# Kernel optimization log

Measured on AMD Instinct MI355X. Metric: run time of the kernel, lower is better.

## Reference

```python
import jax, jax.numpy as jnp
import numpy as np

N_NODES = 100000
NODE_DIM = 64
IN_DIM_V = 128
N_LAYERS = 4
N_CLASSES = 40
N_EDGES = 1600000
LEAKY_SLOPE = 0.2
BN_EPS = 1e-5


def setup_inputs() -> dict:
    key = jax.random.key(0)
    ks = jax.random.split(key, 12)
    V = jax.random.normal(ks[0], (N_NODES, IN_DIM_V), dtype=jnp.float32)
    src = jax.random.randint(ks[1], (N_EDGES,), 0, N_NODES, dtype=jnp.int64 if jax.config.jax_enable_x64 else jnp.int32)
    dst = jax.random.randint(ks[2], (N_EDGES,), 0, N_NODES, dtype=jnp.int64 if jax.config.jax_enable_x64 else jnp.int32)
    s_in = 1.0 / np.sqrt(IN_DIM_V)
    s_h = 1.0 / np.sqrt(NODE_DIM)
    W_in = jax.random.normal(ks[3], (IN_DIM_V, NODE_DIM), dtype=jnp.float32) * s_in
    b_in = jnp.zeros((NODE_DIM,), jnp.float32)
    W_l = jax.random.normal(ks[4], (N_LAYERS, NODE_DIM, NODE_DIM), dtype=jnp.float32) * s_h
    b_l = jnp.zeros((N_LAYERS, NODE_DIM), jnp.float32)
    gamma = jnp.ones((N_LAYERS, NODE_DIM), jnp.float32)
    beta = jnp.zeros((N_LAYERS, NODE_DIM), jnp.float32)
    W_out = jax.random.normal(ks[5], (NODE_DIM, N_CLASSES), dtype=jnp.float32) * s_h
    b_out = jnp.zeros((N_CLASSES,), jnp.float32)
    return {"V": V, "src": src, "dst": dst, "W_in": W_in, "b_in": b_in,
            "W_l": W_l, "b_l": b_l, "gamma": gamma, "beta": beta,
            "W_out": W_out, "b_out": b_out}


def _batchnorm(x, g, b):
    # BatchNorm1d in training mode: biased variance over the node axis
    m = jnp.mean(x, axis=0)
    v = jnp.mean(jnp.square(x - m), axis=0)
    return (x - m) * jax.lax.rsqrt(v + BN_EPS) * g + b


def reference(V, src, dst, W_in, b_in, W_l, b_l, gamma, beta, W_out, b_out):
    N = V.shape[0]
    ones = jnp.ones((src.shape[0],), V.dtype)
    deg_out = jax.ops.segment_sum(ones, src, num_segments=N)
    deg_in = jax.ops.segment_sum(ones, dst, num_segments=N)
    norm_src = jax.lax.rsqrt(jnp.clip(deg_out, 1.0))[:, None]  # [N,1]
    norm_dst = jax.lax.rsqrt(jnp.clip(deg_in, 1.0))[:, None]

    # trans_input: linear embedding in_dim_V -> node_dim
    h = V @ W_in + b_in  # [N, node_dim]

    for l in range(N_LAYERS):
        h_in = h
        # dropout p=0 / eval mode -> identity
        # GraphConv norm='both': D^{-1/2} A D^{-1/2} X W + b
        m = h * norm_src                                      # [N, d]
        agg = jax.ops.segment_sum(m[src], dst, num_segments=N)  # gather-scatter over edges
        agg = agg * norm_dst
        hc = agg @ W_l[l] + b_l[l]
        hc = _batchnorm(hc, gamma[l], beta[l])
        hc = jnp.where(hc >= 0, hc, LEAKY_SLOPE * hc)
        h = hc + h_in  # residual (cell index hard-wired to 1 in source)

    logits = h @ W_out + b_out  # trans_output: node_dim -> n_classes
    return jax.nn.log_softmax(logits, axis=1)
```

## Files before the change

kernel.cpp:

```cpp
#include <hip/hip_runtime.h>
#include <math.h>


#define LEAKY_SLOPE 0.2f
#define BN_EPS 1e-5f
#define DEG_CAP 48

__device__ __forceinline__ unsigned short f2bf(float f) {
  unsigned int x = __float_as_uint(f);
  unsigned int r = (x + 0x7FFFu + ((x >> 16) & 1u)) >> 16;
  return (unsigned short)r;
}
__device__ __forceinline__ float bf2f(unsigned short u) {
  return __uint_as_float((unsigned int)u << 16);
}

__global__ __launch_bounds__(256, 8)
void hist_kernel(const int* __restrict__ src, int* __restrict__ cnt_src, int E, int N) {
  int bid = blockIdx.x;
  int w = bid & 7;
  int chunk = (N + 7) >> 3;
  int lo = w * chunk;
  int hi = min(lo + chunk, N);
  int i = (bid >> 3) * blockDim.x + threadIdx.x;
  int stride = (gridDim.x >> 3) * blockDim.x;
  for (; i < E; i += stride) {
    int s = src[i];
    if (s >= lo && s < hi) atomicAdd(&cnt_src[s], 1);
  }
}

__global__ __launch_bounds__(256, 8)
void fill_kernel(const int* __restrict__ src, const int* __restrict__ dst,
                 int* __restrict__ cnt_dst, int* __restrict__ bucket, int E, int N) {
  int bid = blockIdx.x;
  int w = bid & 7;
  int chunk = (N + 7) >> 3;
  int lo = w * chunk;
  int hi = min(lo + chunk, N);
  int i = (bid >> 3) * blockDim.x + threadIdx.x;
  int stride = (gridDim.x >> 3) * blockDim.x;
  for (; i < E; i += stride) {
    int d = dst[i];
    if (d >= lo && d < hi) {
      int pos = atomicAdd(&cnt_dst[d], 1);
      if (pos < DEG_CAP) bucket[d * DEG_CAP + pos] = src[i];
    }
  }
}

__global__ __launch_bounds__(256, 8)
void norms_kernel(const int* __restrict__ cnt_src, const int* __restrict__ cnt_dst,
                  float* __restrict__ norm_src, float* __restrict__ norm_dst, int N) {
  int i = blockIdx.x * blockDim.x + threadIdx.x;
  if (i < N) {
    norm_src[i] = rsqrtf(fmaxf((float)cnt_src[i], 1.0f));
    norm_dst[i] = rsqrtf(fmaxf((float)cnt_dst[i], 1.0f));
  }
}

__global__ __launch_bounds__(256) __attribute__((amdgpu_waves_per_eu(3, 4)))
void input_gemm_kernel(const float* __restrict__ V, const float* __restrict__ W_in,
                       const float* __restrict__ b_in, const float* __restrict__ norm_src,
                       float* __restrict__ h, unsigned short* __restrict__ hs, int N) {
  __shared__ __align__(16) float sW[128][64];
  __shared__ __align__(16) float sA[32][132];
  int tid = threadIdx.x;
  int c0 = (tid & 15) * 4;
  int rp = tid >> 4;
  int base = blockIdx.x * 32;

  float4 b4 = *(const float4*)&b_in[c0];

  #pragma unroll
  for (int it = 0; it < 8; it++) {
    int i = tid + it * 256;
    int r = i >> 4, cc = (i & 15) * 4;
    *(float4*)&sW[r][cc] = *(const float4*)&W_in[r * 64 + cc];
  }
  #pragma unroll
  for (int it = 0; it < 4; it++) {
    int i = tid + it * 256;
    int r = i >> 5, cc = (i & 31) * 4;
    int n = base + r;
    float4 v = make_float4(0.f, 0.f, 0.f, 0.f);
    if (n < N) v = *(const float4*)&V[(size_t)n * 128 + cc];
    *(float4*)&sA[r][cc] = v;
  }
  __syncthreads();

  int r0 = rp * 2, r1 = rp * 2 + 1;
  float acc0[4] = {0.f, 0.f, 0.f, 0.f};
  float acc1[4] = {0.f, 0.f, 0.f, 0.f};
  #pragma unroll 4
  for (int d0 = 0; d0 < 128; d0 += 4) {
    float4 wr0 = *(const float4*)&sW[d0 + 0][c0];
    float4 wr1 = *(const float4*)&sW[d0 + 1][c0];
    float4 wr2 = *(const float4*)&sW[d0 + 2][c0];
    float4 wr3 = *(const float4*)&sW[d0 + 3][c0];
    float4 a0 = *(const float4*)&sA[r0][d0];
    float4 a1 = *(const float4*)&sA[r1][d0];
    acc0[0] += a0.x * wr0.x + a0.y * wr1.x + a0.z * wr2.x + a0.w * wr3.x;
    acc0[1] += a0.x * wr0.y + a0.y * wr1.y + a0.z * wr2.y + a0.w * wr3.y;
    acc0[2] += a0.x * wr0.z + a0.y * wr1.z + a0.z * wr2.z + a0.w * wr3.z;
    acc0[3] += a0.x * wr0.w + a0.y * wr1.w + a0.z * wr2.w + a0.w * wr3.w;
    acc1[0] += a1.x * wr0.x + a1.y * wr1.x + a1.z * wr2.x + a1.w * wr3.x;
    acc1[1] += a1.x * wr0.y + a1.y * wr1.y + a1.z * wr2.y + a1.w * wr3.y;
    acc1[2] += a1.x * wr0.z + a1.y * wr1.z + a1.z * wr2.z + a1.w * wr3.z;
    acc1[3] += a1.x * wr0.w + a1.y * wr1.w + a1.z * wr2.w + a1.w * wr3.w;
  }

  int n0 = base + r0, n1 = base + r1;
  if (n0 < N) {
    float4 o = make_float4(acc0[0] + b4.x, acc0[1] + b4.y, acc0[2] + b4.z, acc0[3] + b4.w);
    *(float4*)&h[(size_t)n0 * 64 + c0] = o;
    float ns = norm_src[n0];
    ushort4 s = make_ushort4(f2bf(o.x * ns), f2bf(o.y * ns), f2bf(o.z * ns), f2bf(o.w * ns));
    *(ushort4*)&hs[(size_t)n0 * 64 + c0] = s;
  }
  if (n1 < N) {
    float4 o = make_float4(acc1[0] + b4.x, acc1[1] + b4.y, acc1[2] + b4.z, acc1[3] + b4.w);
    *(float4*)&h[(size_t)n1 * 64 + c0] = o;
    float ns = norm_src[n1];
    ushort4 s = make_ushort4(f2bf(o.x * ns), f2bf(o.y * ns), f2bf(o.z * ns), f2bf(o.w * ns));
    *(ushort4*)&hs[(size_t)n1 * 64 + c0] = s;
  }
}

__global__ __launch_bounds__(256, 8)
void agg_kernel(const unsigned short* __restrict__ hs, const float* __restrict__ norm_dst,
                const int* __restrict__ cnt_dst, const int* __restrict__ bucket,
                float* __restrict__ agg, int N) {
  int wid = __builtin_amdgcn_readfirstlane(blockIdx.x * 4 + (threadIdx.x >> 6));
  int lane = threadIdx.x & 63;
  if (wid >= N) return;
  int len = cnt_dst[wid];
  float nd = norm_dst[wid];
  const int* bkt = bucket + wid * DEG_CAP;
  float a0=0.f,a1=0.f,a2=0.f,a3=0.f,a4=0.f,a5=0.f,a6=0.f,a7=0.f;
  for (int j = 0; j < len; j += 8) {
    int s0=0,s1=0,s2=0,s3=0,s4=0,s5=0,s6=0,s7=0;
    if (j + 0 < len) s0 = bkt[j + 0];
    if (j + 1 < len) s1 = bkt[j + 1];
    if (j + 2 < len) s2 = bkt[j + 2];
    if (j + 3 < len) s3 = bkt[j + 3];
    if (j + 4 < len) s4 = bkt[j + 4];
    if (j + 5 < len) s5 = bkt[j + 5];
    if (j + 6 < len) s6 = bkt[j + 6];
    if (j + 7 < len) s7 = bkt[j + 7];
    unsigned short h0=0,h1=0,h2=0,h3=0,h4=0,h5=0,h6=0,h7=0;
    if (j + 0 < len) h0 = hs[(size_t)s0 * 64 + lane];
    if (j + 1 < len) h1 = hs[(size_t)s1 * 64 + lane];
    if (j + 2 < len) h2 = hs[(size_t)s2 * 64 + lane];
    if (j + 3 < len) h3 = hs[(size_t)s3 * 64 + lane];
    if (j + 4 < len) h4 = hs[(size_t)s4 * 64 + lane];
    if (j + 5 < len) h5 = hs[(size_t)s5 * 64 + lane];
    if (j + 6 < len) h6 = hs[(size_t)s6 * 64 + lane];
    if (j + 7 < len) h7 = hs[(size_t)s7 * 64 + lane];
    if (j + 0 < len) a0 += bf2f(h0);
    if (j + 1 < len) a1 += bf2f(h1);
    if (j + 2 < len) a2 += bf2f(h2);
    if (j + 3 < len) a3 += bf2f(h3);
    if (j + 4 < len) a4 += bf2f(h4);
    if (j + 5 < len) a5 += bf2f(h5);
    if (j + 6 < len) a6 += bf2f(h6);
    if (j + 7 < len) a7 += bf2f(h7);
  }
  float acc = ((a0 + a1) + (a2 + a3)) + ((a4 + a5) + (a6 + a7));
  agg[(size_t)wid * 64 + lane] = acc * nd;
}

__global__ __launch_bounds__(256) __attribute__((amdgpu_waves_per_eu(4, 4)))
void gemm_stats_kernel(const float* __restrict__ agg, const float* __restrict__ W,
                       const float* __restrict__ b, float* __restrict__ hc,
                       float* __restrict__ stats, int N) {
  __shared__ __align__(16) float sW[64][64];
  __shared__ __align__(16) float sA[64][68];
  int tid = threadIdx.x;
  int lane = tid & 63;
  int wv = tid >> 6;
  int cg = lane & 15;
  int ng = lane >> 4;
  int nrow0 = wv * 16 + ng * 4;
  int base = blockIdx.x * 64;

  #pragma unroll
  for (int it = 0; it < 4; it++) {
    int i = tid + it * 256;
    int r = i >> 4, c4 = (i & 15) * 4;
    *(float4*)&sW[r][c4] = *(const float4*)&W[r * 64 + c4];
  }
  #pragma unroll
  for (int it = 0; it < 4; it++) {
    int i = tid + it * 256;
    int r = i >> 4, c4 = (i & 15) * 4;
    int n = base + r;
    float4 v = make_float4(0.f, 0.f, 0.f, 0.f);
    if (n < N) v = *(const float4*)&agg[(size_t)n * 64 + c4];
    *(float4*)&sA[r][c4] = v;
  }
  __syncthreads();

  float4 b4 = *(const float4*)&b[cg * 4];

  float acc[4][4];
  #pragma unroll
  for (int i = 0; i < 4; i++)
    #pragma unroll
    for (int c = 0; c < 4; c++) acc[i][c] = 0.f;

  #pragma unroll 4
  for (int d0 = 0; d0 < 64; d0 += 4) {
    float4 wr0 = *(const float4*)&sW[d0 + 0][cg * 4];
    float4 wr1 = *(const float4*)&sW[d0 + 1][cg * 4];
    float4 wr2 = *(const float4*)&sW[d0 + 2][cg * 4];
    float4 wr3 = *(const float4*)&sW[d0 + 3][cg * 4];
    #pragma unroll
    for (int i = 0; i < 4; i++) {
      float4 av = *(const float4*)&sA[nrow0 + i][d0];
      acc[i][0] += av.x * wr0.x + av.y * wr1.x + av.z * wr2.x + av.w * wr3.x;
      acc[i][1] += av.x * wr0.y + av.y * wr1.y + av.z * wr2.y + av.w * wr3.y;
      acc[i][2] += av.x * wr0.z + av.y * wr1.z + av.z * wr2.z + av.w * wr3.z;
      acc[i][3] += av.x * wr0.w + av.y * wr1.w + av.z * wr2.w + av.w * wr3.w;
    }
  }

  float st_s0=0.f,st_s1=0.f,st_s2=0.f,st_s3=0.f;
  float st_q0=0.f,st_q1=0.f,st_q2=0.f,st_q3=0.f;
  #pragma unroll
  for (int i = 0; i < 4; i++) {
    int n = base + nrow0 + i;
    if (n < N) {
      float4 o;
      o.x = acc[i][0] + b4.x; o.y = acc[i][1] + b4.y;
      o.z = acc[i][2] + b4.z; o.w = acc[i][3] + b4.w;
      *(float4*)&hc[(size_t)n * 64 + cg * 4] = o;
      st_s0 += o.x; st_s1 += o.y; st_s2 += o.z; st_s3 += o.w;
      st_q0 += o.x * o.x; st_q1 += o.y * o.y;
      st_q2 += o.z * o.z; st_q3 += o.w * o.w;
    }
  }

  __syncthreads();
  int rr = wv * 4 + ng;
  *(float4*)&sA[rr][cg * 4]      = make_float4(st_s0, st_s1, st_s2, st_s3);
  *(float4*)&sA[16 + rr][cg * 4] = make_float4(st_q0, st_q1, st_q2, st_q3);
  __syncthreads();
  if (tid < 64) {
    float s = 0.f, q = 0.f;
    #pragma unroll
    for (int r = 0; r < 16; r++) { s += sA[r][tid]; q += sA[16 + r][tid]; }
    atomicAdd(&stats[tid], s);
    atomicAdd(&stats[64 + tid], q);
  }
}

__global__ __launch_bounds__(256, 8)
void apply_kernel(const float* __restrict__ hc, const float* __restrict__ stats,
                  const float* __restrict__ gamma, const float* __restrict__ beta,
                  const float* __restrict__ norm_src, float* __restrict__ h,
                  unsigned short* __restrict__ hs, int N, int write_hs) {
  __shared__ float s_scale[64];
  __shared__ float s_shift[64];
  int tid = threadIdx.x;
  if (tid < 64) {
    float s = stats[tid];
    float ss = stats[64 + tid];
    float invN = 1.0f / (float)N;
    float mean = s * invN;
    float var = fmaxf(ss * invN - mean * mean, 0.0f);
    float scale = gamma[tid] * rsqrtf(var + BN_EPS);
    s_scale[tid] = scale;
    s_shift[tid] = beta[tid] - mean * scale;
  }
  __syncthreads();
  int total4 = N * 16;
  int i = blockIdx.x * blockDim.x + threadIdx.x;
  int stride = gridDim.x * blockDim.x;
  for (; i < total4; i += stride) {
    float4 v = ((const float4*)hc)[i];
    float4 r = ((const float4*)h)[i];
    int cb = (i * 4) & 63;
    int n = i >> 4;
    float o0 = v.x * s_scale[cb + 0] + s_shift[cb + 0];
    float o1 = v.y * s_scale[cb + 1] + s_shift[cb + 1];
    float o2 = v.z * s_scale[cb + 2] + s_shift[cb + 2];
    float o3 = v.w * s_scale[cb + 3] + s_shift[cb + 3];
    o0 = (o0 >= 0.f) ? o0 : LEAKY_SLOPE * o0;
    o1 = (o1 >= 0.f) ? o1 : LEAKY_SLOPE * o1;
    o2 = (o2 >= 0.f) ? o2 : LEAKY_SLOPE * o2;
    o3 = (o3 >= 0.f) ? o3 : LEAKY_SLOPE * o3;
    float4 oh;
    oh.x = o0 + r.x; oh.y = o1 + r.y; oh.z = o2 + r.z; oh.w = o3 + r.w;
    ((float4*)h)[i] = oh;
    if (write_hs) {
      float nsc = norm_src[n];
      ushort4 os = make_ushort4(f2bf(oh.x * nsc), f2bf(oh.y * nsc),
                                f2bf(oh.z * nsc), f2bf(oh.w * nsc));
      ((ushort4*)hs)[i] = os;
    }
  }
}

__global__ __launch_bounds__(256, 4)
void out_kernel(const float* __restrict__ h, const float* __restrict__ W_out,
                const float* __restrict__ b_out, float* __restrict__ out, int N) {
  __shared__ float sWoT[40][65];
  int tid = threadIdx.x;
  for (int i = tid; i < 2560; i += 256) {
    int d = i / 40;
    int c = i - d * 40;
    sWoT[c][d] = W_out[i];
  }
  __syncthreads();
  int gw = (int)((blockIdx.x * blockDim.x + tid) >> 6);
  int nw = (int)((gridDim.x * blockDim.x) >> 6);
  int lane = tid & 63;
  int cc = (lane < 40) ? lane : 39;
  float bias = (lane < 40) ? b_out[lane] : 0.f;
  const float* wrow = &sWoT[cc][0];
  for (int n = gw; n < N; n += nw) {
    int nsg = __builtin_amdgcn_readfirstlane(n);
    const float* hrow = h + (size_t)nsg * 64;
    float acc = bias;
    #pragma unroll
    for (int d = 0; d < 64; d++) acc += hrow[d] * wrow[d];
    float lg = (lane < 40) ? acc : -INFINITY;
    float m = lg;
    #pragma unroll
    for (int off = 32; off; off >>= 1) m = fmaxf(m, __shfl_xor(m, off));
    float e = (lane < 40) ? expf(acc - m) : 0.f;
    float s = e;
    #pragma unroll
    for (int off = 32; off; off >>= 1) s += __shfl_xor(s, off);
    float lse = m + logf(s);
    if (lane < 40) out[(size_t)nsg * 40 + lane] = acc - lse;
  }
}

extern "C" void kernel_launch(void* const* d_in, const int* in_sizes, int n_in,
                              void* d_out, int out_size, void* d_ws, size_t ws_size,
                              hipStream_t stream) {
  const float* V     = (const float*)d_in[0];
  const int*   src   = (const int*)d_in[1];
  const int*   dst   = (const int*)d_in[2];
  const float* W_in  = (const float*)d_in[3];
  const float* b_in  = (const float*)d_in[4];
  const float* W_l   = (const float*)d_in[5];
  const float* b_l   = (const float*)d_in[6];
  const float* gamma = (const float*)d_in[7];
  const float* beta  = (const float*)d_in[8];
  const float* W_out = (const float*)d_in[9];
  const float* b_out = (const float*)d_in[10];
  float* out = (float*)d_out;

  const int N = in_sizes[0] / 128;
  const int E = in_sizes[1];
  const int NL = 4;

  char* p = (char*)d_ws;
  auto alloc = [&](size_t bytes) {
    void* r = (void*)p;
    p += (bytes + 255) & ~(size_t)255;
    return r;
  };
  float*          h       = (float*)alloc((size_t)N * 64 * 4);
  float*          agg     = (float*)alloc((size_t)N * 64 * 4);
  float*          hc      = (float*)alloc((size_t)N * 64 * 4);
  unsigned short* hs      = (unsigned short*)alloc((size_t)N * 64 * 2);
  int*            bucket  = (int*)alloc((size_t)N * DEG_CAP * 4);
  int*            cnt_src = (int*)alloc((size_t)N * 4);
  int*            cnt_dst = (int*)alloc((size_t)N * 4);
  float*          nrm_src = (float*)alloc((size_t)N * 4);
  float*          nrm_dst = (float*)alloc((size_t)N * 4);
  float*          stats   = (float*)alloc(128 * 4);
  (void)ws_size;

  hipMemsetAsync(cnt_src, 0, (size_t)N * 4, stream);
  hipMemsetAsync(cnt_dst, 0, (size_t)N * 4, stream);

  hist_kernel<<<2048, 256, 0, stream>>>(src, cnt_src, E, N);
  fill_kernel<<<2048, 256, 0, stream>>>(src, dst, cnt_dst, bucket, E, N);
  norms_kernel<<<(N + 255) / 256, 256, 0, stream>>>(cnt_src, cnt_dst, nrm_src, nrm_dst, N);

  input_gemm_kernel<<<(N + 31) / 32, 256, 0, stream>>>(V, W_in, b_in, nrm_src, h, hs, N);

  for (int l = 0; l < NL; l++) {
    agg_kernel<<<(N + 3) / 4, 256, 0, stream>>>(hs, nrm_dst, cnt_dst, bucket, agg, N);
    hipMemsetAsync(stats, 0, 128 * 4, stream);
    gemm_stats_kernel<<<(N + 63) / 64, 256, 0, stream>>>(agg, W_l + (size_t)l * 64 * 64,
                                                         b_l + (size_t)l * 64, hc, stats, N);
    apply_kernel<<<2048, 256, 0, stream>>>(hc, stats, gamma + (size_t)l * 64,
                                           beta + (size_t)l * 64, nrm_src, h, hs, N,
                                           (l < NL - 1) ? 1 : 0);
  }

  out_kernel<<<1024, 256, 0, stream>>>(h, W_out, b_out, out, N);
}
```

Before: 923.7 us.

## Fuse hist/fill, last apply into output, persistent GEMMs, drop stats memsets

Merges the source-degree histogram and destination bucket fill into one pass over the edge arrays. The final BatchNorm, LeakyReLU and residual step is folded into the output projection and log-softmax kernel, so h is not written back after the last layer. The input and layer GEMMs become grid-stride persistent kernels with 1024 blocks, which amortizes the weight loads into shared memory and cuts the number of stats atomics. The per-layer memsets are replaced by one zeroing of a per-layer stats buffer inside norms_kernel. In exchange, the fused fill does both the src and dst atomics inside each partition pass, and the persistent loops add extra __syncthreads.

```diff
diff --git a/kernel.cpp b/kernel.cpp
--- a/kernel.cpp
+++ b/kernel.cpp
@@ -16,7 +16,9 @@
 }
 
 __global__ __launch_bounds__(256, 8)
-void hist_kernel(const int* __restrict__ src, int* __restrict__ cnt_src, int E, int N) {
+void fill_hist_kernel(const int* __restrict__ src, const int* __restrict__ dst,
+                      int* __restrict__ cnt_src, int* __restrict__ cnt_dst,
+                      int* __restrict__ bucket, int E, int N) {
   int bid = blockIdx.x;
   int w = bid & 7;
   int chunk = (N + 7) >> 3;
@@ -26,33 +28,26 @@
   int stride = (gridDim.x >> 3) * blockDim.x;
   for (; i < E; i += stride) {
     int s = src[i];
+    int d = dst[i];
     if (s >= lo && s < hi) atomicAdd(&cnt_src[s], 1);
-  }
-}
-
-__global__ __launch_bounds__(256, 8)
-void fill_kernel(const int* __restrict__ src, const int* __restrict__ dst,
-                 int* __restrict__ cnt_dst, int* __restrict__ bucket, int E, int N) {
-  int bid = blockIdx.x;
-  int w = bid & 7;
-  int chunk = (N + 7) >> 3;
-  int lo = w * chunk;
-  int hi = min(lo + chunk, N);
-  int i = (bid >> 3) * blockDim.x + threadIdx.x;
-  int stride = (gridDim.x >> 3) * blockDim.x;
-  for (; i < E; i += stride) {
-    int d = dst[i];
     if (d >= lo && d < hi) {
       int pos = atomicAdd(&cnt_dst[d], 1);
-      if (pos < DEG_CAP) bucket[d * DEG_CAP + pos] = src[i];
+      if (pos < DEG_CAP) bucket[d * DEG_CAP + pos] = s;
     }
   }
 }
 
 __global__ __launch_bounds__(256, 8)
 void norms_kernel(const int* __restrict__ cnt_src, const int* __restrict__ cnt_dst,
-                  float* __restrict__ norm_src, float* __restrict__ norm_dst, int N) {
+                  float* __restrict__ norm_src, float* __restrict__ norm_dst,
+                  float* __restrict__ stats, int N) {
   int i = blockIdx.x * blockDim.x + threadIdx.x;
+  if (blockIdx.x == 0) {
+    if (threadIdx.x < 256) {
+      stats[threadIdx.x] = 0.f;
+      stats[256 + threadIdx.x] = 0.f;
+    }
+  }
   if (i < N) {
     norm_src[i] = rsqrtf(fmaxf((float)cnt_src[i], 1.0f));
     norm_dst[i] = rsqrtf(fmaxf((float)cnt_dst[i], 1.0f));
@@ -68,7 +63,6 @@
   int tid = threadIdx.x;
   int c0 = (tid & 15) * 4;
   int rp = tid >> 4;
-  int base = blockIdx.x * 32;
 
   float4 b4 = *(const float4*)&b_in[c0];
 
@@ -78,52 +72,56 @@
     int r = i >> 4, cc = (i & 15) * 4;
     *(float4*)&sW[r][cc] = *(const float4*)&W_in[r * 64 + cc];
   }
-  #pragma unroll
-  for (int it = 0; it < 4; it++) {
-    int i = tid + it * 256;
-    int r = i >> 5, cc = (i & 31) * 4;
-    int n = base + r;
-    float4 v = make_float4(0.f, 0.f, 0.f, 0.f);
-    if (n < N) v = *(const float4*)&V[(size_t)n * 128 + cc];
-    *(float4*)&sA[r][cc] = v;
-  }
-  __syncthreads();
-
-  int r0 = rp * 2, r1 = rp * 2 + 1;
-  float acc0[4] = {0.f, 0.f, 0.f, 0.f};
-  float acc1[4] = {0.f, 0.f, 0.f, 0.f};
-  #pragma unroll 4
-  for (int d0 = 0; d0 < 128; d0 += 4) {
-    float4 wr0 = *(const float4*)&sW[d0 + 0][c0];
-    float4 wr1 = *(const float4*)&sW[d0 + 1][c0];
-    float4 wr2 = *(const float4*)&sW[d0 + 2][c0];
-    float4 wr3 = *(const float4*)&sW[d0 + 3][c0];
-    float4 a0 = *(const float4*)&sA[r0][d0];
-    float4 a1 = *(const float4*)&sA[r1][d0];
-    acc0[0] += a0.x * wr0.x + a0.y * wr1.x + a0.z * wr2.x + a0.w * wr3.x;
-    acc0[1] += a0.x * wr0.y + a0.y * wr1.y + a0.z * wr2.y + a0.w * wr3.y;
-    acc0[2] += a0.x * wr0.z + a0.y * wr1.z + a0.z * wr2.z + a0.w * wr3.z;
-    acc0[3] += a0.x * wr0.w + a0.y * wr1.w + a0.z * wr2.w + a0.w * wr3.w;
-    acc1[0] += a1.x * wr0.x + a1.y * wr1.x + a1.z * wr2.x + a1.w * wr3.x;
-    acc1[1] += a1.x * wr0.y + a1.y * wr1.y + a1.z * wr2.y + a1.w * wr3.y;
-    acc1[2] += a1.x * wr0.z + a1.y * wr1.z + a1.z * wr2.z + a1.w * wr3.z;
-    acc1[3] += a1.x * wr0.w + a1.y * wr1.w + a1.z * wr2.w + a1.w * wr3.w;
-  }
-
-  int n0 = base + r0, n1 = base + r1;
-  if (n0 < N) {
-    float4 o = make_float4(acc0[0] + b4.x, acc0[1] + b4.y, acc0[2] + b4.z, acc0[3] + b4.w);
-    *(float4*)&h[(size_t)n0 * 64 + c0] = o;
-    float ns = norm_src[n0];
-    ushort4 s = make_ushort4(f2bf(o.x * ns), f2bf(o.y * ns), f2bf(o.z * ns), f2bf(o.w * ns));
-    *(ushort4*)&hs[(size_t)n0 * 64 + c0] = s;
-  }
-  if (n1 < N) {
-    float4 o = make_float4(acc1[0] + b4.x, acc1[1] + b4.y, acc1[2] + b4.z, acc1[3] + b4.w);
-    *(float4*)&h[(size_t)n1 * 64 + c0] = o;
-    float ns = norm_src[n1];
-    ushort4 s = make_ushort4(f2bf(o.x * ns), f2bf(o.y * ns), f2bf(o.z * ns), f2bf(o.w * ns));
-    *(ushort4*)&hs[(size_t)n1 * 64 + c0] = s;
+
+  for (int base = blockIdx.x * 32; base < N; base += gridDim.x * 32) {
+    __syncthreads();
+    #pragma unroll
+    for (int it = 0; it < 4; it++) {
+      int i = tid + it * 256;
+      int r = i >> 5, cc = (i & 31) * 4;
+      int n = base + r;
+      float4 v = make_float4(0.f, 0.f, 0.f, 0.f);
+      if (n < N) v = *(const float4*)&V[(size_t)n * 128 + cc];
+      *(float4*)&sA[r][cc] = v;
+    }
+    __syncthreads();
+
+    int r0 = rp * 2, r1 = rp * 2 + 1;
+    float acc0[4] = {0.f, 0.f, 0.f, 0.f};
+    float acc1[4] = {0.f, 0.f, 0.f, 0.f};
+    #pragma unroll 4
+    for (int d0 = 0; d0 < 128; d0 += 4) {
+      float4 wr0 = *(const float4*)&sW[d0 + 0][c0];
+      float4 wr1 = *(const float4*)&sW[d0 + 1][c0];
+      float4 wr2 = *(const float4*)&sW[d0 + 2][c0];
+      float4 wr3 = *(const float4*)&sW[d0 + 3][c0];
+      float4 a0 = *(const float4*)&sA[r0][d0];
+      float4 a1 = *(const float4*)&sA[r1][d0];
+      acc0[0] += a0.x * wr0.x + a0.y * wr1.x + a0.z * wr2.x + a0.w * wr3.x;
+      acc0[1] += a0.x * wr0.y + a0.y * wr1.y + a0.z * wr2.y + a0.w * wr3.y;
+      acc0[2] += a0.x * wr0.z + a0.y * wr1.z + a0.z * wr2.z + a0.w * wr3.z;
+      acc0[3] += a0.x * wr0.w + a0.y * wr1.w + a0.z * wr2.w + a0.w * wr3.w;
+      acc1[0] += a1.x * wr0.x + a1.y * wr1.x + a1.z * wr2.x + a1.w * wr3.x;
+      acc1[1] += a1.x * wr0.y + a1.y * wr1.y + a1.z * wr2.y + a1.w * wr3.y;
+      acc1[2] += a1.x * wr0.z + a1.y * wr1.z + a1.z * wr2.z + a1.w * wr3.z;
+      acc1[3] += a1.x * wr0.w + a1.y * wr1.w + a1.z * wr2.w + a1.w * wr3.w;
+    }
+
+    int n0 = base + r0, n1 = base + r1;
+    if (n0 < N) {
+      float4 o = make_float4(acc0[0] + b4.x, acc0[1] + b4.y, acc0[2] + b4.z, acc0[3] + b4.w);
+      *(float4*)&h[(size_t)n0 * 64 + c0] = o;
+      float ns = norm_src[n0];
+      ushort4 s = make_ushort4(f2bf(o.x * ns), f2bf(o.y * ns), f2bf(o.z * ns), f2bf(o.w * ns));
+      *(ushort4*)&hs[(size_t)n0 * 64 + c0] = s;
+    }
+    if (n1 < N) {
+      float4 o = make_float4(acc1[0] + b4.x, acc1[1] + b4.y, acc1[2] + b4.z, acc1[3] + b4.w);
+      *(float4*)&h[(size_t)n1 * 64 + c0] = o;
+      float ns = norm_src[n1];
+      ushort4 s = make_ushort4(f2bf(o.x * ns), f2bf(o.y * ns), f2bf(o.z * ns), f2bf(o.w * ns));
+      *(ushort4*)&hs[(size_t)n1 * 64 + c0] = s;
+    }
   }
 }
 
@@ -182,7 +180,6 @@
   int cg = lane & 15;
   int ng = lane >> 4;
   int nrow0 = wv * 16 + ng * 4;
-  int base = blockIdx.x * 64;
 
   #pragma unroll
   for (int it = 0; it < 4; it++) {
@@ -190,54 +187,59 @@
     int r = i >> 4, c4 = (i & 15) * 4;
     *(float4*)&sW[r][c4] = *(const float4*)&W[r * 64 + c4];
   }
-  #pragma unroll
-  for (int it = 0; it < 4; it++) {
-    int i = tid + it * 256;
-    int r = i >> 4, c4 = (i & 15) * 4;
-    int n = base + r;
-    float4 v = make_float4(0.f, 0.f, 0.f, 0.f);
-    if (n < N) v = *(const float4*)&agg[(size_t)n * 64 + c4];
-    *(float4*)&sA[r][c4] = v;
-  }
-  __syncthreads();
 
   float4 b4 = *(const float4*)&b[cg * 4];
-
-  float acc[4][4];
-  #pragma unroll
-  for (int i = 0; i < 4; i++)
-    #pragma unroll
-    for (int c = 0; c < 4; c++) acc[i][c] = 0.f;
-
-  #pragma unroll 4
-  for (int d0 = 0; d0 < 64; d0 += 4) {
-    float4 wr0 = *(const float4*)&sW[d0 + 0][cg * 4];
-    float4 wr1 = *(const float4*)&sW[d0 + 1][cg * 4];
-    float4 wr2 = *(const float4*)&sW[d0 + 2][cg * 4];
-    float4 wr3 = *(const float4*)&sW[d0 + 3][cg * 4];
-    #pragma unroll
-    for (int i = 0; i < 4; i++) {
-      float4 av = *(const float4*)&sA[nrow0 + i][d0];
-      acc[i][0] += av.x * wr0.x + av.y * wr1.x + av.z * wr2.x + av.w * wr3.x;
-      acc[i][1] += av.x * wr0.y + av.y * wr1.y + av.z * wr2.y + av.w * wr3.y;
-      acc[i][2] += av.x * wr0.z + av.y * wr1.z + av.z * wr2.z + av.w * wr3.z;
-      acc[i][3] += av.x * wr0.w + av.y * wr1.w + av.z * wr2.w + av.w * wr3.w;
-    }
-  }
 
   float st_s0=0.f,st_s1=0.f,st_s2=0.f,st_s3=0.f;
   float st_q0=0.f,st_q1=0.f,st_q2=0.f,st_q3=0.f;
-  #pragma unroll
-  for (int i = 0; i < 4; i++) {
-    int n = base + nrow0 + i;
-    if (n < N) {
-      float4 o;
-      o.x = acc[i][0] + b4.x; o.y = acc[i][1] + b4.y;
-      o.z = acc[i][2] + b4.z; o.w = acc[i][3] + b4.w;
-      *(float4*)&hc[(size_t)n * 64 + cg * 4] = o;
-      st_s0 += o.x; st_s1 += o.y; st_s2 += o.z; st_s3 += o.w;
-      st_q0 += o.x * o.x; st_q1 += o.y * o.y;
-      st_q2 += o.z * o.z; st_q3 += o.w * o.w;
+
+  for (int base = blockIdx.x * 64; base < N; base += gridDim.x * 64) {
+    __syncthreads();
+    #pragma unroll
+    for (int it = 0; it < 4; it++) {
+      int i = tid + it * 256;
+      int r = i >> 4, c4 = (i & 15) * 4;
+      int n = base + r;
+      float4 v = make_float4(0.f, 0.f, 0.f, 0.f);
+      if (n < N) v = *(const float4*)&agg[(size_t)n * 64 + c4];
+      *(float4*)&sA[r][c4] = v;
+    }
+    __syncthreads();
+
+    float acc[4][4];
+    #pragma unroll
+    for (int i = 0; i < 4; i++)
+      #pragma unroll
+      for (int c = 0; c < 4; c++) acc[i][c] = 0.f;
+
+    #pragma unroll 4
+    for (int d0 = 0; d0 < 64; d0 += 4) {
+      float4 wr0 = *(const float4*)&sW[d0 + 0][cg * 4];
+      float4 wr1 = *(const float4*)&sW[d0 + 1][cg * 4];
+      float4 wr2 = *(const float4*)&sW[d0 + 2][cg * 4];
+      float4 wr3 = *(const float4*)&sW[d0 + 3][cg * 4];
+      #pragma unroll
+      for (int i = 0; i < 4; i++) {
+        float4 av = *(const float4*)&sA[nrow0 + i][d0];
+        acc[i][0] += av.x * wr0.x + av.y * wr1.x + av.z * wr2.x + av.w * wr3.x;
+        acc[i][1] += av.x * wr0.y + av.y * wr1.y + av.z * wr2.y + av.w * wr3.y;
+        acc[i][2] += av.x * wr0.z + av.y * wr1.z + av.z * wr2.z + av.w * wr3.z;
+        acc[i][3] += av.x * wr0.w + av.y * wr1.w + av.z * wr2.w + av.w * wr3.w;
+      }
+    }
+
+    #pragma unroll
+    for (int i = 0; i < 4; i++) {
+      int n = base + nrow0 + i;
+      if (n < N) {
+        float4 o;
+        o.x = acc[i][0] + b4.x; o.y = acc[i][1] + b4.y;
+        o.z = acc[i][2] + b4.z; o.w = acc[i][3] + b4.w;
+        *(float4*)&hc[(size_t)n * 64 + cg * 4] = o;
+        st_s0 += o.x; st_s1 += o.y; st_s2 += o.z; st_s3 += o.w;
+        st_q0 += o.x * o.x; st_q1 += o.y * o.y;
+        st_q2 += o.z * o.z; st_q3 += o.w * o.w;
+      }
     }
   }
 
@@ -259,7 +261,7 @@
 void apply_kernel(const float* __restrict__ hc, const float* __restrict__ stats,
                   const float* __restrict__ gamma, const float* __restrict__ beta,
                   const float* __restrict__ norm_src, float* __restrict__ h,
-                  unsigned short* __restrict__ hs, int N, int write_hs) {
+                  unsigned short* __restrict__ hs, int N) {
   __shared__ float s_scale[64];
   __shared__ float s_shift[64];
   int tid = threadIdx.x;
@@ -293,38 +295,55 @@
     float4 oh;
     oh.x = o0 + r.x; oh.y = o1 + r.y; oh.z = o2 + r.z; oh.w = o3 + r.w;
     ((float4*)h)[i] = oh;
-    if (write_hs) {
-      float nsc = norm_src[n];
-      ushort4 os = make_ushort4(f2bf(oh.x * nsc), f2bf(oh.y * nsc),
-                                f2bf(oh.z * nsc), f2bf(oh.w * nsc));
-      ((ushort4*)hs)[i] = os;
-    }
+    float nsc = norm_src[n];
+    ushort4 os = make_ushort4(f2bf(oh.x * nsc), f2bf(oh.y * nsc),
+                              f2bf(oh.z * nsc), f2bf(oh.w * nsc));
+    ((ushort4*)hs)[i] = os;
   }
 }
 
 __global__ __launch_bounds__(256, 4)
-void out_kernel(const float* __restrict__ h, const float* __restrict__ W_out,
-                const float* __restrict__ b_out, float* __restrict__ out, int N) {
+void out_fused_kernel(const float* __restrict__ hc, const float* __restrict__ stats,
+                      const float* __restrict__ gamma, const float* __restrict__ beta,
+                      const float* __restrict__ h, const float* __restrict__ W_out,
+                      const float* __restrict__ b_out, float* __restrict__ out, int N) {
   __shared__ float sWoT[40][65];
+  __shared__ float s_scale[64];
+  __shared__ float s_shift[64];
+  __shared__ float sH[4][64];
   int tid = threadIdx.x;
   for (int i = tid; i < 2560; i += 256) {
     int d = i / 40;
     int c = i - d * 40;
     sWoT[c][d] = W_out[i];
   }
+  if (tid < 64) {
+    float s = stats[tid];
+    float ss = stats[64 + tid];
+    float invN = 1.0f / (float)N;
+    float mean = s * invN;
+    float var = fmaxf(ss * invN - mean * mean, 0.0f);
+    float scale = gamma[tid] * rsqrtf(var + BN_EPS);
+    s_scale[tid] = scale;
+    s_shift[tid] = beta[tid] - mean * scale;
+  }
   __syncthreads();
-  int gw = (int)((blockIdx.x * blockDim.x + tid) >> 6);
-  int nw = (int)((gridDim.x * blockDim.x) >> 6);
+  int wv = tid >> 6;
   int lane = tid & 63;
+  int gw = blockIdx.x * 4 + wv;
+  int nw = gridDim.x * 4;
   int cc = (lane < 40) ? lane : 39;
   float bias = (lane < 40) ? b_out[lane] : 0.f;
-  const float* wrow = &sWoT[cc][0];
   for (int n = gw; n < N; n += nw) {
-    int nsg = __builtin_amdgcn_readfirstlane(n);
-    const float* hrow = h + (size_t)nsg * 64;
+    float v = hc[(size_t)n * 64 + lane];
+    float o = v * s_scale[lane] + s_shift[lane];
+    o = (o >= 0.f) ? o : LEAKY_SLOPE * o;
+    float oh = o + h[(size_t)n * 64 + lane];
+    sH[wv][lane] = oh;
+    __builtin_amdgcn_wave_barrier();
     float acc = bias;
     #pragma unroll
-    for (int d = 0; d < 64; d++) acc += hrow[d] * wrow[d];
+    for (int d = 0; d < 64; d++) acc += sH[wv][d] * sWoT[cc][d];
     float lg = (lane < 40) ? acc : -INFINITY;
     float m = lg;
     #pragma unroll
@@ -334,7 +353,8 @@
     #pragma unroll
     for (int off = 32; off; off >>= 1) s += __shfl_xor(s, off);
     float lse = m + logf(s);
-    if (lane < 40) out[(size_t)nsg * 40 + lane] = acc - lse;
+    if (lane < 40) out[(size_t)n * 40 + lane] = acc - lse;
+    __builtin_amdgcn_wave_barrier();
   }
 }
 
@@ -373,27 +393,30 @@
   int*            cnt_dst = (int*)alloc((size_t)N * 4);
   float*          nrm_src = (float*)alloc((size_t)N * 4);
   float*          nrm_dst = (float*)alloc((size_t)N * 4);
-  float*          stats   = (float*)alloc(128 * 4);
+  float*          stats   = (float*)alloc(4 * 128 * 4);
   (void)ws_size;
 
   hipMemsetAsync(cnt_src, 0, (size_t)N * 4, stream);
   hipMemsetAsync(cnt_dst, 0, (size_t)N * 4, stream);
 
-  hist_kernel<<<2048, 256, 0, stream>>>(src, cnt_src, E, N);
-  fill_kernel<<<2048, 256, 0, stream>>>(src, dst, cnt_dst, bucket, E, N);
-  norms_kernel<<<(N + 255) / 256, 256, 0, stream>>>(cnt_src, cnt_dst, nrm_src, nrm_dst, N);
-
-  input_gemm_kernel<<<(N + 31) / 32, 256, 0, stream>>>(V, W_in, b_in, nrm_src, h, hs, N);
+  fill_hist_kernel<<<2048, 256, 0, stream>>>(src, dst, cnt_src, cnt_dst, bucket, E, N);
+  norms_kernel<<<(N + 255) / 256, 256, 0, stream>>>(cnt_src, cnt_dst, nrm_src, nrm_dst,
+                                                    stats, N);
+
+  input_gemm_kernel<<<1024, 256, 0, stream>>>(V, W_in, b_in, nrm_src, h, hs, N);
 
   for (int l = 0; l < NL; l++) {
+    float* statl = stats + (size_t)l * 128;
     agg_kernel<<<(N + 3) / 4, 256, 0, stream>>>(hs, nrm_dst, cnt_dst, bucket, agg, N);
-    hipMemsetAsync(stats, 0, 128 * 4, stream);
-    gemm_stats_kernel<<<(N + 63) / 64, 256, 0, stream>>>(agg, W_l + (size_t)l * 64 * 64,
-                                                         b_l + (size_t)l * 64, hc, stats, N);
-    apply_kernel<<<2048, 256, 0, stream>>>(hc, stats, gamma + (size_t)l * 64,
-                                           beta + (size_t)l * 64, nrm_src, h, hs, N,
-                                           (l < NL - 1) ? 1 : 0);
-  }
-
-  out_kernel<<<1024, 256, 0, stream>>>(h, W_out, b_out, out, N);
-}
+    gemm_stats_kernel<<<1024, 256, 0, stream>>>(agg, W_l + (size_t)l * 64 * 64,
+                                                b_l + (size_t)l * 64, hc, statl, N);
+    if (l < NL - 1) {
+      apply_kernel<<<2048, 256, 0, stream>>>(hc, statl, gamma + (size_t)l * 64,
+                                             beta + (size_t)l * 64, nrm_src, h, hs, N);
+    } else {
+      out_fused_kernel<<<2048, 256, 0, stream>>>(hc, statl, gamma + (size_t)l * 64,
+                                                 beta + (size_t)l * 64, h, W_out,
+                                                 b_out, out, N);
+    }
+  }
+}
```

After: 893.0 us. -3.3%, faster.
